# Performance work log

Measured on AMD Instinct MI355X. Metric: run time of the kernel, lower is better.

Reference implementation:

```python
import jax, jax.numpy as jnp
import numpy as np

R = 2            # kernel_radius
N_IN = 64
N_OUT = 128
H, W = 209, 133  # input spatial dims (NHWC)
KH, KW = 4 * R + 1, 2 * R + 1


def hex_indices(radius):
    """Coordinates of hexagon cells inside a (4r+1, 2r+1) grid."""
    moves = np.array([[1, 1], [2, 0], [1, -1], [-1, -1], [-2, 0], [-1, 1]])
    out = [[2 * radius, radius]]
    for il in range(1, radius + 1):
        s = np.array([[2 * radius - 2 * il, radius]])
        cur = moves.repeat(il, axis=0).cumsum(axis=0)
        out.extend((s + cur).tolist())
    return np.array(out, dtype=np.int32)


def make_out_mask(h, w, r):
    out_h, out_w = h - 4 * r, w - 2 * r
    mr = (out_w - 1) // 2  # hex radius of the output mask
    f = np.zeros((mr * 4 + 1, mr * 2 + 1), dtype=np.float32)
    for ind in hex_indices(mr):
        f[tuple(ind)] = 1.0
    i_cut = (mr * 4 + 1 - out_h) // 2
    f = f[i_cut:-i_cut, :]
    return f.reshape(out_h, out_w, 1)


_HEX = hex_indices(R)               # [19, 2]
_N_IND = _HEX.shape[0]
# scatter indices matching MakeVariableIndices ordering:
# for ci in range(N_IN): for co in range(N_OUT): for j in range(n_ind)
_HW = np.tile(_HEX, (N_IN * N_OUT, 1))                       # [19*Nin*Nout, 2]
_CI = np.repeat(np.arange(N_IN), _N_IND * N_OUT)
_CO = np.tile(np.repeat(np.arange(N_OUT), _N_IND), N_IN)
_OUT_MASK = jnp.asarray(make_out_mask(H, W, R))              # [201, 129, 1]


def setup_inputs() -> dict:
    key = jax.random.key(0)
    k1, k2, k3 = jax.random.split(key, 3)
    # glorot-normal-ish scale for the sparse kernel weights
    fan = _N_IND * (N_IN + N_OUT) / 2.0
    sparse_weights = jax.random.normal(k1, (_N_IND * N_IN * N_OUT,), jnp.float32) * np.sqrt(1.0 / fan).astype(np.float32)
    x = jax.random.normal(k2, (16, H, W, N_IN), jnp.float32)
    offset = jax.random.normal(k3, (1, 1, 1, N_OUT), jnp.float32) * 0.1
    return {"x": x, "sparse_weights": sparse_weights, "offset": offset}


def reference(x, sparse_weights, offset):
    # rebuild dense hex-masked kernel [KH, KW, N_IN, N_OUT]
    kernel = jnp.zeros((KH, KW, N_IN, N_OUT), dtype=sparse_weights.dtype)
    kernel = kernel.at[_HW[:, 0], _HW[:, 1], _CI, _CO].set(sparse_weights)
    conv = jax.lax.conv_general_dilated(
        x, kernel, window_strides=(1, 1), padding="VALID",
        dimension_numbers=("NHWC", "HWIO", "NHWC"))
    return jax.nn.elu(conv + offset) * _OUT_MASK
```

## Files before the change

kernel.cpp:

```cpp
#include <hip/hip_runtime.h>
#include <math.h>

#define NB   16
#define HH   209
#define WW   133
#define CIN  64
#define COUT 128
#define OH   201
#define OW   129
#define NTAP 19
#define NW   (NTAP*CIN*COUT)

#define XS 72

typedef __attribute__((ext_vector_type(8))) __bf16 bf16x8;
typedef __attribute__((ext_vector_type(4))) float f32x4;
typedef __attribute__((ext_vector_type(4))) unsigned short us4;

__device__ __forceinline__ unsigned short f2bf(float f) {
  unsigned int u = __builtin_bit_cast(unsigned int, f);
  u += 0x7FFFu + ((u >> 16) & 1u);
  return (unsigned short)(u >> 16);
}

__global__ __launch_bounds__(256) void repack_w(const float* __restrict__ w,
                                                unsigned short* __restrict__ wt) {
  int gid = blockIdx.x * 256 + threadIdx.x;
  int ci = gid & 63;
  int co = (gid >> 6) & 127;
  int k  = gid >> 13;
  wt[gid] = f2bf(w[ci * (COUT * NTAP) + co * NTAP + k]);
}

__global__ __launch_bounds__(256) void conv_hex_mfma(const float* __restrict__ x,
                                                     const unsigned short* __restrict__ wt,
                                                     const float* __restrict__ offs,
                                                     float* __restrict__ out) {
  constexpr int c_start[9] = {0, 1, 3, 6, 8, 11, 13, 16, 18};
  constexpr int c_cnt[9]   = {1, 2, 3, 2, 3, 2, 3, 2, 1};
  constexpr int c_k[19]  = {18, 7,17, 6, 8,16, 1, 5, 0, 9,15, 2, 4, 3,10,14, 11,13, 12};
  constexpr int c_dw[19] = { 2, 3, 1, 2, 4, 0, 3, 1, 2, 4, 0, 3, 1, 2, 4, 0, 3, 1, 2};

  __shared__ unsigned short xs[2][82 * XS];

  const int tid  = threadIdx.x;
  const int lane = tid & 63;
  const int wv   = tid >> 6;
  const int l15  = lane & 15;
  const int quad = lane >> 4;
  const int n0   = wv * 32;

  const int bid = blockIdx.x;
  const int oi  = bid % OH;
  const int b   = bid / OH;
  const int par = oi & 1;
  const int na  = 65 - par;

  int ad = oi - 100; ad = ad < 0 ? -ad : ad;
  const int lim = 128 - ad;

  int a_lo_raw = 64 - lim - par;
  int a_lo = a_lo_raw <= 0 ? 0 : (a_lo_raw + 1) >> 1;
  int a_hi = (64 + lim - par) >> 1;
  if (a_hi > na - 1) a_hi = na - 1;

  const int f0 = a_lo >> 4;
  const int f1 = a_hi >> 4;
  const int nf = f1 - f0 + 1;
  const int p0 = f0 * 16;
  const int npos   = nf * 16;
  const int nchunk = (npos + 2) * 16;

  float* outb = out + (size_t)(b * OH + oi) * OW * COUT;

  {
    const float4 z = make_float4(0.f, 0.f, 0.f, 0.f);
    const int opar = par ^ 1;
    const int nopp = 65 - opar;
    for (int idx = tid; idx < nopp * 32; idx += 256) {
      int q  = idx >> 5;
      int c4 = idx & 31;
      *(float4*)(outb + (size_t)(opar + 2 * q) * COUT + c4 * 4) = z;
    }
    const int hi_start = p0 + npos;
    const int hi_cnt   = na > hi_start ? na - hi_start : 0;
    const int tot      = (p0 + hi_cnt) * 32;
    for (int idx = tid; idx < tot; idx += 256) {
      int q  = idx >> 5;
      int a  = q < p0 ? q : hi_start + (q - p0);
      int c4 = idx & 31;
      *(float4*)(outb + (size_t)(par + 2 * a) * COUT + c4 * 4) = z;
    }
  }

  f32x4 acc[5][2];
  #pragma unroll
  for (int i = 0; i < 5; ++i)
    #pragma unroll
    for (int j = 0; j < 2; ++j) acc[i][j] = (f32x4){0.f, 0.f, 0.f, 0.f};

  const float* xb = x + (size_t)b * (HH * WW * CIN);

  float4 stg[6];
  bf16x8 bfrag[3][2][2];

  auto load_stg = [&](int r) {
    const float* xr = xb + (size_t)(oi + r) * (WW * CIN);
    const int rpar = (par + r) & 1;
    #pragma unroll
    for (int i = 0; i < 6; ++i) {
      int c = tid + i * 256;
      if (c < nchunk) {
        int j  = c >> 4;
        int c4 = c & 15;
        int col = rpar + 2 * (p0 + j);
        if (col > WW - 1) col = WW - 1;
        stg[i] = *(const float4*)(xr + (size_t)col * CIN + c4 * 4);
      }
    }
  };
  auto store_stg = [&](int buf) {
    #pragma unroll
    for (int i = 0; i < 6; ++i) {
      int c = tid + i * 256;
      if (c < nchunk) {
        int j  = c >> 4;
        int c4 = c & 15;
        us4 o;
        o.x = f2bf(stg[i].x); o.y = f2bf(stg[i].y);
        o.z = f2bf(stg[i].z); o.w = f2bf(stg[i].w);
        *(us4*)(&xs[buf][j * XS + c4 * 4]) = o;
      }
    }
  };

  load_stg(0);
  store_stg(0);

  #pragma unroll
  for (int r = 0; r < 9; ++r) {
    {
      const int st = c_start[r], cnt = c_cnt[r];
      #pragma unroll
      for (int t = 0; t < 3; ++t) {
        if (t < cnt) {
          const unsigned short* wb = wt + (size_t)c_k[st + t] * (CIN * COUT);
          #pragma unroll
          for (int j = 0; j < 2; ++j) {
            const unsigned short* wn = wb + (size_t)(n0 + j * 16 + l15) * CIN + quad * 8;
            bfrag[t][0][j] = *(const bf16x8*)(wn);
            bfrag[t][1][j] = *(const bf16x8*)(wn + 32);
          }
        }
      }
    }
    if (r < 8) load_stg(r + 1);
    __syncthreads();

    {
      const int st = c_start[r], cnt = c_cnt[r];
      const unsigned short* bufp = xs[r & 1];
      #pragma unroll
      for (int t = 0; t < 3; ++t) {
        if (t < cnt) {
          const int s = (par + c_dw[st + t]) >> 1;
          #pragma unroll
          for (int ks = 0; ks < 2; ++ks) {
            #pragma unroll
            for (int mf = 0; mf < 5; ++mf) {
              if (mf < nf) {
                bf16x8 a = *(const bf16x8*)(&bufp[(mf * 16 + l15 + s) * XS + ks * 32 + quad * 8]);
                acc[mf][0] = __builtin_amdgcn_mfma_f32_16x16x32_bf16(a, bfrag[t][ks][0], acc[mf][0], 0, 0, 0);
                acc[mf][1] = __builtin_amdgcn_mfma_f32_16x16x32_bf16(a, bfrag[t][ks][1], acc[mf][1], 0, 0, 0);
              }
            }
          }
        }
      }
    }

    if (r < 8) store_stg((r + 1) & 1);
  }

  const float off0 = offs[n0 + l15];
  const float off1 = offs[n0 + 16 + l15];
  #pragma unroll
  for (int mf = 0; mf < 5; ++mf) {
    if (mf < nf) {
      #pragma unroll
      for (int r = 0; r < 4; ++r) {
        int a  = (f0 + mf) * 16 + quad * 4 + r;
        int oj = par + 2 * a;
        if (oj <= OW - 1) {
          int adj = oj - 64; adj = adj < 0 ? -adj : adj;
          bool valid = adj <= lim;
          float v0 = acc[mf][0][r] + off0;
          float v1 = acc[mf][1][r] + off1;
          float e0 = v0 > 0.f ? v0 : expm1f(v0);
          float e1 = v1 > 0.f ? v1 : expm1f(v1);
          outb[(size_t)oj * COUT + n0 + l15]      = valid ? e0 : 0.f;
          outb[(size_t)oj * COUT + n0 + 16 + l15] = valid ? e1 : 0.f;
        }
      }
    }
  }
}

extern "C" void kernel_launch(void* const* d_in, const int* in_sizes, int n_in,
                              void* d_out, int out_size, void* d_ws, size_t ws_size,
                              hipStream_t stream) {
  const float* x   = (const float*)d_in[0];
  const float* sw  = (const float*)d_in[1];
  const float* off = (const float*)d_in[2];
  float* out = (float*)d_out;

  unsigned short* wtb = (unsigned short*)d_ws;
  repack_w<<<NW / 256, 256, 0, stream>>>(sw, wtb);
  conv_hex_mfma<<<NB * OH, 256, 0, stream>>>(x, wtb, off, out);
}
```

Baseline: 416.5 us.

## Compute three output rows per block to reuse staged input rows

Each block now handles three consecutive output rows (67 tiles per image) instead of one, so every input row staged in LDS is used for up to three output rows, with three accumulator sets. This cuts the global reads and bf16 conversion of input rows roughly threefold. The costs are a larger register footprint (a launch_bounds occupancy hint was added), weight fragments re-fetched from global/L2 for the second and third rows, a union column range across rows that may do some wasted MFMA work, and a third as many blocks.

After: 498.7 us. 1.2x slower.

```diff
diff --git a/kernel.cpp b/kernel.cpp
--- a/kernel.cpp
+++ b/kernel.cpp
@@ -10,6 +10,8 @@
 #define OW   129
 #define NTAP 19
 #define NW   (NTAP*CIN*COUT)
+#define OT   3
+#define NTILE 67
 
 #define XS 72
 
@@ -32,10 +34,10 @@
   wt[gid] = f2bf(w[ci * (COUT * NTAP) + co * NTAP + k]);
 }
 
-__global__ __launch_bounds__(256) void conv_hex_mfma(const float* __restrict__ x,
-                                                     const unsigned short* __restrict__ wt,
-                                                     const float* __restrict__ offs,
-                                                     float* __restrict__ out) {
+__global__ __launch_bounds__(256, 2) void conv_hex_mfma(const float* __restrict__ x,
+                                                        const unsigned short* __restrict__ wt,
+                                                        const float* __restrict__ offs,
+                                                        float* __restrict__ out) {
   constexpr int c_start[9] = {0, 1, 3, 6, 8, 11, 13, 16, 18};
   constexpr int c_cnt[9]   = {1, 2, 3, 2, 3, 2, 3, 2, 1};
   constexpr int c_k[19]  = {18, 7,17, 6, 8,16, 1, 5, 0, 9,15, 2, 4, 3,10,14, 11,13, 12};
@@ -50,54 +52,70 @@
   const int quad = lane >> 4;
   const int n0   = wv * 32;
 
-  const int bid = blockIdx.x;
-  const int oi  = bid % OH;
-  const int b   = bid / OH;
-  const int par = oi & 1;
-  const int na  = 65 - par;
-
-  int ad = oi - 100; ad = ad < 0 ? -ad : ad;
-  const int lim = 128 - ad;
-
-  int a_lo_raw = 64 - lim - par;
-  int a_lo = a_lo_raw <= 0 ? 0 : (a_lo_raw + 1) >> 1;
-  int a_hi = (64 + lim - par) >> 1;
-  if (a_hi > na - 1) a_hi = na - 1;
-
-  const int f0 = a_lo >> 4;
-  const int f1 = a_hi >> 4;
-  const int nf = f1 - f0 + 1;
-  const int p0 = f0 * 16;
-  const int npos   = nf * 16;
+  const int bid  = blockIdx.x;
+  const int tile = bid % NTILE;
+  const int b    = bid / NTILE;
+  const int oi0  = tile * OT;
+  const int par0 = oi0 & 1;
+
+  int limt[OT];
+  int f0u = 7, f1u = 0;
+  #pragma unroll
+  for (int t = 0; t < OT; ++t) {
+    const int oi = oi0 + t;
+    const int p  = (par0 + t) & 1;
+    int ad = oi - 100; ad = ad < 0 ? -ad : ad;
+    const int L = 128 - ad;
+    limt[t] = L;
+    const int na = 65 - p;
+    int alr = 64 - L - p;
+    int alo = alr <= 0 ? 0 : (alr + 1) >> 1;
+    int ahi = (64 + L - p) >> 1;
+    if (ahi > na - 1) ahi = na - 1;
+    const int f0 = alo >> 4;
+    const int f1 = ahi >> 4;
+    f0u = f0 < f0u ? f0 : f0u;
+    f1u = f1 > f1u ? f1 : f1u;
+  }
+  const int nfu    = f1u - f0u + 1;
+  const int p0     = f0u * 16;
+  const int npos   = nfu * 16;
   const int nchunk = (npos + 2) * 16;
-
-  float* outb = out + (size_t)(b * OH + oi) * OW * COUT;
 
   {
     const float4 z = make_float4(0.f, 0.f, 0.f, 0.f);
-    const int opar = par ^ 1;
-    const int nopp = 65 - opar;
-    for (int idx = tid; idx < nopp * 32; idx += 256) {
-      int q  = idx >> 5;
-      int c4 = idx & 31;
-      *(float4*)(outb + (size_t)(opar + 2 * q) * COUT + c4 * 4) = z;
-    }
-    const int hi_start = p0 + npos;
-    const int hi_cnt   = na > hi_start ? na - hi_start : 0;
-    const int tot      = (p0 + hi_cnt) * 32;
-    for (int idx = tid; idx < tot; idx += 256) {
-      int q  = idx >> 5;
-      int a  = q < p0 ? q : hi_start + (q - p0);
-      int c4 = idx & 31;
-      *(float4*)(outb + (size_t)(par + 2 * a) * COUT + c4 * 4) = z;
-    }
-  }
-
-  f32x4 acc[5][2];
+    for (int t = 0; t < OT; ++t) {
+      float* outb = out + (size_t)((b * OH) + oi0 + t) * OW * COUT;
+      const int p    = (par0 + t) & 1;
+      const int opar = p ^ 1;
+      const int nopp = 65 - opar;
+      for (int idx = tid; idx < nopp * 32; idx += 256) {
+        int q  = idx >> 5;
+        int c4 = idx & 31;
+        *(float4*)(outb + (size_t)(opar + 2 * q) * COUT + c4 * 4) = z;
+      }
+      const int na = 65 - p;
+      const int hi_start = p0 + npos;
+      const int hi_cnt   = na > hi_start ? na - hi_start : 0;
+      const int tot      = (p0 + hi_cnt) * 32;
+      for (int idx = tid; idx < tot; idx += 256) {
+        int q  = idx >> 5;
+        int a  = q < p0 ? q : hi_start + (q - p0);
+        int c4 = idx & 31;
+        *(float4*)(outb + (size_t)(p + 2 * a) * COUT + c4 * 4) = z;
+      }
+    }
+  }
+
+  f32x4 acc0[5][2], acc1[5][2], acc2[5][2];
   #pragma unroll
   for (int i = 0; i < 5; ++i)
     #pragma unroll
-    for (int j = 0; j < 2; ++j) acc[i][j] = (f32x4){0.f, 0.f, 0.f, 0.f};
+    for (int j = 0; j < 2; ++j) {
+      acc0[i][j] = (f32x4){0.f, 0.f, 0.f, 0.f};
+      acc1[i][j] = (f32x4){0.f, 0.f, 0.f, 0.f};
+      acc2[i][j] = (f32x4){0.f, 0.f, 0.f, 0.f};
+    }
 
   const float* xb = x + (size_t)b * (HH * WW * CIN);
 
@@ -105,8 +123,8 @@
   bf16x8 bfrag[3][2][2];
 
   auto load_stg = [&](int r) {
-    const float* xr = xb + (size_t)(oi + r) * (WW * CIN);
-    const int rpar = (par + r) & 1;
+    const float* xr = xb + (size_t)(oi0 + r) * (WW * CIN);
+    const int rpar = (par0 + r) & 1;
     #pragma unroll
     for (int i = 0; i < 6; ++i) {
       int c = tid + i * 256;
@@ -134,72 +152,98 @@
     }
   };
 
+  auto compute_row = [&](f32x4 (&accR)[5][2], int r, int pt,
+                         const unsigned short* bufp, bool usePre) {
+    const int st = c_start[r], cnt = c_cnt[r];
+    #pragma unroll
+    for (int t = 0; t < 3; ++t) {
+      if (t < cnt) {
+        bf16x8 b0[2], b1[2];
+        if (usePre) {
+          b0[0] = bfrag[t][0][0]; b0[1] = bfrag[t][0][1];
+          b1[0] = bfrag[t][1][0]; b1[1] = bfrag[t][1][1];
+        } else {
+          const unsigned short* wb = wt + (size_t)c_k[st + t] * (CIN * COUT);
+          #pragma unroll
+          for (int jj = 0; jj < 2; ++jj) {
+            const unsigned short* wn = wb + (size_t)(n0 + jj * 16 + l15) * CIN + quad * 8;
+            b0[jj] = *(const bf16x8*)(wn);
+            b1[jj] = *(const bf16x8*)(wn + 32);
+          }
+        }
+        const int s = (pt + c_dw[st + t]) >> 1;
+        #pragma unroll
+        for (int mf = 0; mf < 5; ++mf) {
+          if (mf < nfu) {
+            const unsigned short* ap = &bufp[(mf * 16 + l15 + s) * XS + quad * 8];
+            bf16x8 a0 = *(const bf16x8*)(ap);
+            bf16x8 a1 = *(const bf16x8*)(ap + 32);
+            accR[mf][0] = __builtin_amdgcn_mfma_f32_16x16x32_bf16(a0, b0[0], accR[mf][0], 0, 0, 0);
+            accR[mf][1] = __builtin_amdgcn_mfma_f32_16x16x32_bf16(a0, b0[1], accR[mf][1], 0, 0, 0);
+            accR[mf][0] = __builtin_amdgcn_mfma_f32_16x16x32_bf16(a1, b1[0], accR[mf][0], 0, 0, 0);
+            accR[mf][1] = __builtin_amdgcn_mfma_f32_16x16x32_bf16(a1, b1[1], accR[mf][1], 0, 0, 0);
+          }
+        }
+      }
+    }
+  };
+
   load_stg(0);
   store_stg(0);
 
-  #pragma unroll
-  for (int r = 0; r < 9; ++r) {
-    {
-      const int st = c_start[r], cnt = c_cnt[r];
+  #pragma unroll 1
+  for (int j = 0; j < OT + 8; ++j) {
+    if (j <= 8) {
+      const int st = c_start[j], cnt = c_cnt[j];
       #pragma unroll
       for (int t = 0; t < 3; ++t) {
         if (t < cnt) {
           const unsigned short* wb = wt + (size_t)c_k[st + t] * (CIN * COUT);
           #pragma unroll
-          for (int j = 0; j < 2; ++j) {
-            const unsigned short* wn = wb + (size_t)(n0 + j * 16 + l15) * CIN + quad * 8;
-            bfrag[t][0][j] = *(const bf16x8*)(wn);
-            bfrag[t][1][j] = *(const bf16x8*)(wn + 32);
-          }
-        }
-      }
-    }
-    if (r < 8) load_stg(r + 1);
+          for (int jj = 0; jj < 2; ++jj) {
+            const unsigned short* wn = wb + (size_t)(n0 + jj * 16 + l15) * CIN + quad * 8;
+            bfrag[t][0][jj] = *(const bf16x8*)(wn);
+            bfrag[t][1][jj] = *(const bf16x8*)(wn + 32);
+          }
+        }
+      }
+    }
+    if (j < OT + 7) load_stg(j + 1);
     __syncthreads();
-
-    {
-      const int st = c_start[r], cnt = c_cnt[r];
-      const unsigned short* bufp = xs[r & 1];
-      #pragma unroll
-      for (int t = 0; t < 3; ++t) {
-        if (t < cnt) {
-          const int s = (par + c_dw[st + t]) >> 1;
-          #pragma unroll
-          for (int ks = 0; ks < 2; ++ks) {
-            #pragma unroll
-            for (int mf = 0; mf < 5; ++mf) {
-              if (mf < nf) {
-                bf16x8 a = *(const bf16x8*)(&bufp[(mf * 16 + l15 + s) * XS + ks * 32 + quad * 8]);
-                acc[mf][0] = __builtin_amdgcn_mfma_f32_16x16x32_bf16(a, bfrag[t][ks][0], acc[mf][0], 0, 0, 0);
-                acc[mf][1] = __builtin_amdgcn_mfma_f32_16x16x32_bf16(a, bfrag[t][ks][1], acc[mf][1], 0, 0, 0);
-              }
-            }
-          }
-        }
-      }
-    }
-
-    if (r < 8) store_stg((r + 1) & 1);
+    const unsigned short* bufp = xs[j & 1];
+
+    if (j <= 8)           compute_row(acc0, j,     par0,     bufp, true);
+    if (j >= 1 && j <= 9) compute_row(acc1, j - 1, par0 ^ 1, bufp, false);
+    if (j >= 2)           compute_row(acc2, j - 2, par0,     bufp, false);
+
+    if (j < OT + 7) store_stg((j + 1) & 1);
   }
 
   const float off0 = offs[n0 + l15];
   const float off1 = offs[n0 + 16 + l15];
   #pragma unroll
-  for (int mf = 0; mf < 5; ++mf) {
-    if (mf < nf) {
-      #pragma unroll
-      for (int r = 0; r < 4; ++r) {
-        int a  = (f0 + mf) * 16 + quad * 4 + r;
-        int oj = par + 2 * a;
-        if (oj <= OW - 1) {
-          int adj = oj - 64; adj = adj < 0 ? -adj : adj;
-          bool valid = adj <= lim;
-          float v0 = acc[mf][0][r] + off0;
-          float v1 = acc[mf][1][r] + off1;
-          float e0 = v0 > 0.f ? v0 : expm1f(v0);
-          float e1 = v1 > 0.f ? v1 : expm1f(v1);
-          outb[(size_t)oj * COUT + n0 + l15]      = valid ? e0 : 0.f;
-          outb[(size_t)oj * COUT + n0 + 16 + l15] = valid ? e1 : 0.f;
+  for (int t = 0; t < OT; ++t) {
+    f32x4 (&accR)[5][2] = (t == 0) ? acc0 : ((t == 1) ? acc1 : acc2);
+    float* outb = out + (size_t)((b * OH) + oi0 + t) * OW * COUT;
+    const int pt = (par0 + t) & 1;
+    const int Lt = limt[t];
+    #pragma unroll
+    for (int mf = 0; mf < 5; ++mf) {
+      if (mf < nfu) {
+        #pragma unroll
+        for (int rr = 0; rr < 4; ++rr) {
+          int a  = (f0u + mf) * 16 + quad * 4 + rr;
+          int oj = pt + 2 * a;
+          if (oj <= OW - 1) {
+            int adj = oj - 64; adj = adj < 0 ? -adj : adj;
+            bool valid = adj <= Lt;
+            float v0 = accR[mf][0][rr] + off0;
+            float v1 = accR[mf][1][rr] + off1;
+            float e0 = v0 > 0.f ? v0 : expm1f(v0);
+            float e1 = v1 > 0.f ? v1 : expm1f(v1);
+            outb[(size_t)oj * COUT + n0 + l15]      = valid ? e0 : 0.f;
+            outb[(size_t)oj * COUT + n0 + 16 + l15] = valid ? e1 : 0.f;
+          }
         }
       }
     }
@@ -216,5 +260,5 @@
 
   unsigned short* wtb = (unsigned short*)d_ws;
   repack_w<<<NW / 256, 256, 0, stream>>>(sw, wtb);
-  conv_hex_mfma<<<NB * OH, 256, 0, stream>>>(x, wtb, off, out);
-}
+  conv_hex_mfma<<<NB * NTILE, 256, 0, stream>>>(x, wtb, off, out);
+}
```
